# Kernel optimization log

Hardware: AMD Instinct MI355X
Metric: run time of the kernel (lower is better)

Reference implementation:

```python
import jax, jax.numpy as jnp
import numpy as np

B = 1048576
D = 48
D3 = ((D - 1) // 3 + 1) * 3  # 48
NB = D3 // 3                 # 16 blocks


def setup_inputs() -> dict:
    key = jax.random.key(0)
    k1, k2, k3, k4, k5 = jax.random.split(key, 5)
    rho_real = jax.random.normal(k1, (B, 2, 2), dtype=jnp.float32)
    rho_imag = jax.random.normal(k2, (B, 2, 2), dtype=jnp.float32)
    x = jax.random.normal(k3, (B, D), dtype=jnp.float32)
    w = jax.random.normal(k4, (D,), dtype=jnp.float32) * np.float32(np.sqrt(2.0 / 3.0))
    theta = jax.random.normal(k5, (D3,), dtype=jnp.float32) * np.float32(0.1)
    return {"rho_real": rho_real, "rho_imag": rho_imag, "x": x, "w": w, "theta": theta}


def _apply_blocks(rho, phi):
    # phi: [B, D3]; rho: [B, 2, 2] complex64
    phi_blocks = phi.reshape(phi.shape[0], NB, 3).transpose(1, 0, 2)  # [NB, B, 3]

    def step(r, p):
        a = p[:, 0] * 0.5                       # rotation half-angle
        b = (p[:, 1] + p[:, 2]) * 0.5           # sum phase
        c = (p[:, 1] - p[:, 2]) * 0.5           # diff phase
        ca, sa = jnp.cos(a), jnp.sin(a)
        eb = jnp.exp(1j * b)                    # complex64
        ec = jnp.exp(1j * c)
        row0 = jnp.stack([ca * eb, -sa * ec], axis=-1)
        row1 = jnp.stack([sa * jnp.conj(ec), ca * jnp.conj(eb)], axis=-1)
        U = jnp.stack([row0, row1], axis=-2)    # [B, 2, 2]
        r = jnp.einsum('bim,bmn,bjn->bij', U, r, jnp.conj(U))
        return r, None

    rho, _ = jax.lax.scan(step, rho, phi_blocks)
    return rho


def reference(rho_real, rho_imag, x, w, theta):
    rho = (rho_real + 1j * rho_imag).astype(jnp.complex64)  # [B,2,2]
    wx = x * w                                              # einsum 'j,bj->bj'
    phi = theta[None, :] + jnp.pad(wx, ((0, 0), (0, D3 - D)))
    return _apply_blocks(rho, phi)
```

## Files before the change

### kernel.cpp

```cpp
#include <hip/hip_runtime.h>

#define BLK 256
#define DD  48
#define NB  16

__device__ __forceinline__ float2 cmul(float2 a, float2 b) {
    return make_float2(fmaf(a.x, b.x, -a.y * b.y),
                       fmaf(a.x, b.y,  a.y * b.x));
}
__device__ __forceinline__ float2 cmadd(float2 a, float2 b, float2 c) {
    return make_float2(fmaf(a.x, b.x, fmaf(-a.y, b.y, c.x)),
                       fmaf(a.x, b.y, fmaf( a.y, b.x, c.y)));
}

__global__ __launch_bounds__(BLK) void qlayer_kernel(
    const float* __restrict__ rho_real,
    const float* __restrict__ rho_imag,
    const float* __restrict__ x,
    const float* __restrict__ w,
    const float* __restrict__ theta,
    float* __restrict__ out,
    long long n,
    long long out_floats)
{
    const long long b = (long long)blockIdx.x * BLK + threadIdx.x;
    if (b >= n) return;

    float4 rr = reinterpret_cast<const float4*>(rho_real)[b];
    float4 ri = reinterpret_cast<const float4*>(rho_imag)[b];
    float2 r00 = make_float2(rr.x, ri.x);
    float2 r01 = make_float2(rr.y, ri.y);
    float2 r10 = make_float2(rr.z, ri.z);
    float2 r11 = make_float2(rr.w, ri.w);

    const float4* __restrict__ xv = reinterpret_cast<const float4*>(x + b * DD);

    #pragma unroll
    for (int g = 0; g < 4; ++g) {
        float4 q0 = xv[3 * g + 0];
        float4 q1 = xv[3 * g + 1];
        float4 q2 = xv[3 * g + 2];
        float xs[12] = {q0.x, q0.y, q0.z, q0.w,
                        q1.x, q1.y, q1.z, q1.w,
                        q2.x, q2.y, q2.z, q2.w};
        #pragma unroll
        for (int r = 0; r < 4; ++r) {
            const int j = 12 * g + 3 * r;
            float p0 = fmaf(xs[3 * r + 0], w[j + 0], theta[j + 0]);
            float p1 = fmaf(xs[3 * r + 1], w[j + 1], theta[j + 1]);
            float p2 = fmaf(xs[3 * r + 2], w[j + 2], theta[j + 2]);

            float a  = 0.5f * p0;
            float bb = 0.5f * (p1 + p2);
            float cc = 0.5f * (p1 - p2);
            float sa, ca, sb, cb, sc, ccv;
            __sincosf(a,  &sa, &ca);
            __sincosf(bb, &sb, &cb);
            __sincosf(cc, &sc, &ccv);

            float cacb = ca * cb, casb = ca * sb;
            float sacc = sa * ccv, sasc = sa * sc;
            float2 u00 = make_float2( cacb,  casb);
            float2 u01 = make_float2(-sacc, -sasc);
            float2 u10 = make_float2( sacc, -sasc);
            float2 u11 = make_float2( cacb, -casb);

            float2 t00 = cmadd(u01, r10, cmul(u00, r00));
            float2 t01 = cmadd(u01, r11, cmul(u00, r01));
            float2 t10 = cmadd(u11, r10, cmul(u10, r00));
            float2 t11 = cmadd(u11, r11, cmul(u10, r01));

            float2 cu00 = make_float2(u00.x, -u00.y);
            float2 cu01 = make_float2(u01.x, -u01.y);
            float2 cu10 = make_float2(u10.x, -u10.y);
            float2 cu11 = make_float2(u11.x, -u11.y);
            r00 = cmadd(t01, cu01, cmul(t00, cu00));
            r01 = cmadd(t01, cu11, cmul(t00, cu10));
            r10 = cmadd(t11, cu01, cmul(t10, cu00));
            r11 = cmadd(t11, cu11, cmul(t10, cu10));
        }
    }

    if (4 * b + 4 <= out_floats) {
        reinterpret_cast<float4*>(out)[b] = make_float4(r00.x, r01.x, r10.x, r11.x);
    } else {
        float vals[4] = {r00.x, r01.x, r10.x, r11.x};
        for (int j = 0; j < 4; ++j) {
            long long o = 4 * b + j;
            if (o < out_floats) out[o] = vals[j];
        }
    }
}

extern "C" void kernel_launch(void* const* d_in, const int* in_sizes, int n_in,
                              void* d_out, int out_size, void* d_ws, size_t ws_size,
                              hipStream_t stream) {
    const float* rho_real = (const float*)d_in[0];
    const float* rho_imag = (const float*)d_in[1];
    const float* x        = (const float*)d_in[2];
    const float* w        = (const float*)d_in[3];
    const float* theta    = (const float*)d_in[4];
    float* out = (float*)d_out;

    long long nB = (long long)in_sizes[0] / 4;
    long long nX = (long long)in_sizes[2] / DD;
    long long n  = nB < nX ? nB : nX;
    if (n <= 0) return;

    int grid = (int)((n + BLK - 1) / BLK);
    qlayer_kernel<<<dim3(grid), dim3(BLK), 0, stream>>>(
        rho_real, rho_imag, x, w, theta, out, n, (long long)out_size);
}
```

Before: 317.0 us.

## Rewrite density-matrix conjugation as Bloch-vector rotations

Replaces the explicit 2x2 complex U·rho·U† products with an equivalent Pauli/Bloch-vector form, so each block becomes three real plane rotations on complex Bloch components. This removes most of the complex multiply-add arithmetic per block and drops the half-angle scaling. Only the real part of the output is needed, and it is reconstructed from the trace term and the rotated vector at the end. The kernel is probably memory-bound on reading x, so the smaller ALU load may matter less than it appears.

```diff
diff --git a/kernel.cpp b/kernel.cpp
--- a/kernel.cpp
+++ b/kernel.cpp
@@ -2,16 +2,6 @@
 
 #define BLK 256
 #define DD  48
-#define NB  16
-
-__device__ __forceinline__ float2 cmul(float2 a, float2 b) {
-    return make_float2(fmaf(a.x, b.x, -a.y * b.y),
-                       fmaf(a.x, b.y,  a.y * b.x));
-}
-__device__ __forceinline__ float2 cmadd(float2 a, float2 b, float2 c) {
-    return make_float2(fmaf(a.x, b.x, fmaf(-a.y, b.y, c.x)),
-                       fmaf(a.x, b.y, fmaf( a.y, b.x, c.y)));
-}
 
 __global__ __launch_bounds__(BLK) void qlayer_kernel(
     const float* __restrict__ rho_real,
@@ -28,10 +18,11 @@
 
     float4 rr = reinterpret_cast<const float4*>(rho_real)[b];
     float4 ri = reinterpret_cast<const float4*>(rho_imag)[b];
-    float2 r00 = make_float2(rr.x, ri.x);
-    float2 r01 = make_float2(rr.y, ri.y);
-    float2 r10 = make_float2(rr.z, ri.z);
-    float2 r11 = make_float2(rr.w, ri.w);
+
+    float a0r = 0.5f * (rr.x + rr.w);
+    float v1r = 0.5f * (rr.y + rr.z), v1i = 0.5f * (ri.y + ri.z);
+    float v2r = 0.5f * (ri.z - ri.y), v2i = 0.5f * (rr.y - rr.z);
+    float v3r = 0.5f * (rr.x - rr.w), v3i = 0.5f * (ri.x - ri.w);
 
     const float4* __restrict__ xv = reinterpret_cast<const float4*>(x + b * DD);
 
@@ -50,41 +41,33 @@
             float p1 = fmaf(xs[3 * r + 1], w[j + 1], theta[j + 1]);
             float p2 = fmaf(xs[3 * r + 2], w[j + 2], theta[j + 2]);
 
-            float a  = 0.5f * p0;
-            float bb = 0.5f * (p1 + p2);
-            float cc = 0.5f * (p1 - p2);
-            float sa, ca, sb, cb, sc, ccv;
-            __sincosf(a,  &sa, &ca);
-            __sincosf(bb, &sb, &cb);
-            __sincosf(cc, &sc, &ccv);
+            float s0, c0, s1, c1, s2, c2;
+            __sincosf(p0, &s0, &c0);
+            __sincosf(p1, &s1, &c1);
+            __sincosf(p2, &s2, &c2);
 
-            float cacb = ca * cb, casb = ca * sb;
-            float sacc = sa * ccv, sasc = sa * sc;
-            float2 u00 = make_float2( cacb,  casb);
-            float2 u01 = make_float2(-sacc, -sasc);
-            float2 u10 = make_float2( sacc, -sasc);
-            float2 u11 = make_float2( cacb, -casb);
-
-            float2 t00 = cmadd(u01, r10, cmul(u00, r00));
-            float2 t01 = cmadd(u01, r11, cmul(u00, r01));
-            float2 t10 = cmadd(u11, r10, cmul(u10, r00));
-            float2 t11 = cmadd(u11, r11, cmul(u10, r01));
-
-            float2 cu00 = make_float2(u00.x, -u00.y);
-            float2 cu01 = make_float2(u01.x, -u01.y);
-            float2 cu10 = make_float2(u10.x, -u10.y);
-            float2 cu11 = make_float2(u11.x, -u11.y);
-            r00 = cmadd(t01, cu01, cmul(t00, cu00));
-            r01 = cmadd(t01, cu11, cmul(t00, cu10));
-            r10 = cmadd(t11, cu01, cmul(t10, cu00));
-            r11 = cmadd(t11, cu11, cmul(t10, cu10));
+            float n1r = fmaf(c2, v1r,  s2 * v2r);
+            float n1i = fmaf(c2, v1i,  s2 * v2i);
+            float n2r = fmaf(c2, v2r, -s2 * v1r);
+            float n2i = fmaf(c2, v2i, -s2 * v1i);
+            float m1r = fmaf(c0, n1r,  s0 * v3r);
+            float m1i = fmaf(c0, n1i,  s0 * v3i);
+            float m3r = fmaf(c0, v3r, -s0 * n1r);
+            float m3i = fmaf(c0, v3i, -s0 * n1i);
+            v1r = fmaf(c1, m1r,  s1 * n2r);
+            v1i = fmaf(c1, m1i,  s1 * n2i);
+            v2r = fmaf(c1, n2r, -s1 * m1r);
+            v2i = fmaf(c1, n2i, -s1 * m1i);
+            v3r = m3r;
+            v3i = m3i;
         }
     }
 
     if (4 * b + 4 <= out_floats) {
-        reinterpret_cast<float4*>(out)[b] = make_float4(r00.x, r01.x, r10.x, r11.x);
+        reinterpret_cast<float4*>(out)[b] =
+            make_float4(a0r + v3r, v1r + v2i, v1r - v2i, a0r - v3r);
     } else {
-        float vals[4] = {r00.x, r01.x, r10.x, r11.x};
+        float vals[4] = {a0r + v3r, v1r + v2i, v1r - v2i, a0r - v3r};
         for (int j = 0; j < 4; ++j) {
             long long o = 4 * b + j;
             if (o < out_floats) out[o] = vals[j];
```

New measurement: 311.0 us. Within noise of the previous version (-1.9%).
